# Performance work log

Measured on AMD Instinct MI355X. Metric: run time of the kernel, lower is better.

Reference implementation:

```python
import jax, jax.numpy as jnp
import numpy as np

PAD_IDX, SOS_IDX, EOS_IDX = 0, 1, 2
NEG = -10000.0
B, T, K = 512, 1024, 64


def setup_inputs() -> dict:
    key = jax.random.key(0)
    k1, k2 = jax.random.split(key)
    h = jax.random.normal(k1, (B, T, K), dtype=jnp.float32)
    trans = np.asarray(jax.random.normal(k2, (K, K), dtype=jnp.float32)).copy()
    # constraints applied in crf.__init__
    trans[SOS_IDX, :] = NEG
    trans[:, EOS_IDX] = NEG
    trans[:, PAD_IDX] = NEG
    trans[PAD_IDX, :] = NEG
    trans[PAD_IDX, EOS_IDX] = 0.0
    trans[PAD_IDX, PAD_IDX] = 0.0
    # gold tag sequences: y0[:,0]=SOS, real tags in [3,K), PAD after length
    rng = np.random.default_rng(0)
    lengths = rng.integers(T // 2, T + 1, size=B)
    y = rng.integers(3, K, size=(B, T + 1))
    y[:, 0] = SOS_IDX
    pos = np.arange(1, T + 1)[None, :]
    y[:, 1:] = np.where(pos <= lengths[:, None], y[:, 1:], PAD_IDX)
    return {"h": h, "trans": jnp.asarray(trans), "y0": jnp.asarray(y, dtype=jnp.int64)}


def reference(h, trans, y0):
    mask = (y0[:, 1:] > PAD_IDX).astype(h.dtype)  # [B,T]
    hm = h * mask[:, :, None]                      # rnn.forward masks emissions

    # ---- forward algorithm: log partition Z ----
    init = jnp.full((B, K), NEG, hm.dtype).at[:, SOS_IDX].set(0.0)

    def step(score, xs):
        h_t, m_t = xs  # [B,K], [B]
        # score_t[b, next, prev] = score[b, prev] + h_t[b, next] + trans[next, prev]
        s = jax.nn.logsumexp(score[:, None, :] + h_t[:, :, None] + trans[None], axis=2)
        m = m_t[:, None]
        return s * m + score * (1.0 - m), None

    score, _ = jax.lax.scan(step, init, (hm.transpose(1, 0, 2), mask.T))
    Z = jax.nn.logsumexp(score + trans[EOS_IDX], axis=1)  # [B]

    # ---- gold path score ----
    emit = jnp.take_along_axis(hm, y0[:, 1:, None], axis=2)[..., 0]  # [B,T]
    tr = trans[y0[:, 1:], y0[:, :-1]]                                 # [B,T]
    gold = jnp.sum((emit + tr) * mask, axis=1)
    last_idx = mask.sum(1).astype(jnp.int32)[:, None]                 # length L -> y0[:, L]
    last_tag = jnp.take_along_axis(y0, last_idx.astype(y0.dtype), axis=1)[:, 0]
    gold = gold + trans[EOS_IDX, last_tag]

    return jnp.mean(Z - gold)
```

## Files before the change

### kernel.cpp

```cpp
#include <hip/hip_runtime.h>


#define PAD_IDX 0
#define SOS_IDX 1
#define EOS_IDX 2
constexpr int B = 512, T = 1024, K = 64;
constexpr int REFL = 3;

__device__ __forceinline__ int yval(const int* __restrict__ y, int i, int sh) {
  return y[i << sh];
}

__global__ __launch_bounds__(256) void gold_len_kernel(
    const float* __restrict__ h, const float* __restrict__ trans,
    const int* __restrict__ y0, double* __restrict__ goldOut,
    int* __restrict__ lenOut)
{
  const int b = blockIdx.x, tid = threadIdx.x;
  const float* hb = h + (size_t)b * T * K;
  const int sh = (y0[1] == 0) ? 1 : 0;
  const int* yb = y0 + (((size_t)b * (T + 1)) << sh);

  double acc = 0.0;
  int maxpos = 0;
  for (int t = tid; t < T; t += 256) {
    int ycur = yval(yb, t + 1, sh);
    if (ycur > PAD_IDX) {
      int yprev = yval(yb, t, sh);
      acc += (double)(hb[(size_t)t * K + ycur] + trans[ycur * K + yprev]);
      maxpos = t + 1;
    }
  }
  #pragma unroll
  for (int off = 32; off > 0; off >>= 1) {
    acc += __shfl_down(acc, off, 64);
    maxpos = max(maxpos, __shfl_down(maxpos, off, 64));
  }
  __shared__ double sacc[4];
  __shared__ int smax[4];
  if ((tid & 63) == 0) { sacc[tid >> 6] = acc; smax[tid >> 6] = maxpos; }
  __syncthreads();
  if (tid == 0) {
    double a = (sacc[0] + sacc[1]) + (sacc[2] + sacc[3]);
    int len = max(max(smax[0], smax[1]), max(smax[2], smax[3]));
    int last = yval(yb, len, sh);
    a += (double)trans[EOS_IDX * K + last];
    goldOut[b] = a;
    lenOut[b] = len;
  }
}

__global__ __launch_bounds__(64) void fwd_kernel(
    const float* __restrict__ h, const float* __restrict__ trans,
    const int* __restrict__ lenIn, double* __restrict__ ZdOut)
{
  __shared__ alignas(16) float u_lds[K];
  const int b = blockIdx.x;
  const int k = threadIdx.x;
  const float* hb = h + (size_t)b * T * K;
  const int len = lenIn[b];

  float Er[K];
  #pragma unroll
  for (int j = 0; j < K; ++j) Er[j] = __expf(trans[k * K + j]);

  float u = (k == SOS_IDX) ? 1.0f : 0.0f;
  double O = 0.0;

  auto STEP = [&](float ehv, bool RN) {
    u_lds[k] = u;
    const float4* u4 = reinterpret_cast<const float4*>(u_lds);
    float a[8] = {0, 0, 0, 0, 0, 0, 0, 0};
    #pragma unroll
    for (int c = 0; c < 16; ++c) {
      float4 uu = u4[c];
      a[(4 * c + 0) & 7] = fmaf(Er[4 * c + 0], uu.x, a[(4 * c + 0) & 7]);
      a[(4 * c + 1) & 7] = fmaf(Er[4 * c + 1], uu.y, a[(4 * c + 1) & 7]);
      a[(4 * c + 2) & 7] = fmaf(Er[4 * c + 2], uu.z, a[(4 * c + 2) & 7]);
      a[(4 * c + 3) & 7] = fmaf(Er[4 * c + 3], uu.w, a[(4 * c + 3) & 7]);
    }
    float v = ((a[0] + a[4]) + (a[1] + a[5])) + ((a[2] + a[6]) + (a[3] + a[7]));
    if (RN) {
      float vr = __uint_as_float(__builtin_amdgcn_readlane(__float_as_uint(v), REFL));
      float rc = __builtin_amdgcn_rcpf(vr);
      O -= (double)__logf(rc);
      u = v * rc * ehv;
    } else {
      u = v * ehv;
    }
  };

  const int lm1 = len - 1;
  auto hload = [&](int t) { return hb[(size_t)min(t, lm1) * K + k]; };

  float p0 = hload(0), p1 = hload(1), p2 = hload(2), p3 = hload(3);
  int t = 0;
  for (; t + 4 <= len; t += 4) {
    float n0 = hload(t + 4), n1 = hload(t + 5), n2 = hload(t + 6), n3 = hload(t + 7);
    float e0 = __expf(p0), e1 = __expf(p1), e2 = __expf(p2), e3 = __expf(p3);
    STEP(e0, false); STEP(e1, true); STEP(e2, false); STEP(e3, true);
    p0 = n0; p1 = n1; p2 = n2; p3 = n3;
  }
  for (; t < len; ++t) STEP(__expf(hb[(size_t)t * K + k]), true);

  float w = u * __expf(trans[EOS_IDX * K + k]);
  #pragma unroll
  for (int off = 32; off > 0; off >>= 1) w += __shfl_xor(w, off, 64);
  if (k == 0) ZdOut[b] = O + (double)__logf(w);
}

__global__ __launch_bounds__(512) void reduce_kernel(
    const double* __restrict__ Zd, const double* __restrict__ goldIn,
    float* __restrict__ out)
{
  __shared__ double sdata[8];
  const int tid = threadIdx.x;
  double v = Zd[tid] - goldIn[tid];
  #pragma unroll
  for (int off = 32; off > 0; off >>= 1) v += __shfl_down(v, off, 64);
  if ((tid & 63) == 0) sdata[tid >> 6] = v;
  __syncthreads();
  if (tid == 0) {
    double s = 0.0;
    #pragma unroll
    for (int i = 0; i < 8; ++i) s += sdata[i];
    out[0] = (float)(s / (double)B);
  }
}

extern "C" void kernel_launch(void* const* d_in, const int* in_sizes, int n_in,
                              void* d_out, int out_size, void* d_ws, size_t ws_size,
                              hipStream_t stream) {
  const float* h = (const float*)d_in[0];
  const float* trans = (const float*)d_in[1];
  const int* y0 = (const int*)d_in[2];

  double* Zd = (double*)d_ws;
  double* gold = Zd + B;
  int* len = (int*)(gold + B);

  gold_len_kernel<<<B, 256, 0, stream>>>(h, trans, y0, gold, len);
  fwd_kernel<<<B, 64, 0, stream>>>(h, trans, len, Zd);
  reduce_kernel<<<1, 512, 0, stream>>>(Zd, gold, (float*)d_out);
}
```

Before: 447.0 us.

## Interleave two batch recurrences per wavefront with packed FMA and per-step renormalisation

The forward kernel now gives each 64-lane block two sequences and interleaves their recurrences so the two independent dependency chains hide each other's LDS and FMA latency. It uses packed v2f FMAs and renormalises on every step, guarding against a zero reference value. The gold kernel is widened to 1024 threads so each thread handles one timestep. The cost is half as many blocks and a serial tail for the longer of the two sequences.

```diff
diff --git a/kernel.cpp b/kernel.cpp
--- a/kernel.cpp
+++ b/kernel.cpp
@@ -7,11 +7,13 @@
 constexpr int B = 512, T = 1024, K = 64;
 constexpr int REFL = 3;
 
+typedef float v2f __attribute__((ext_vector_type(2)));
+
 __device__ __forceinline__ int yval(const int* __restrict__ y, int i, int sh) {
   return y[i << sh];
 }
 
-__global__ __launch_bounds__(256) void gold_len_kernel(
+__global__ __launch_bounds__(1024) void gold_len_kernel(
     const float* __restrict__ h, const float* __restrict__ trans,
     const int* __restrict__ y0, double* __restrict__ goldOut,
     int* __restrict__ lenOut)
@@ -21,92 +23,163 @@
   const int sh = (y0[1] == 0) ? 1 : 0;
   const int* yb = y0 + (((size_t)b * (T + 1)) << sh);
 
+  int ycur = yval(yb, tid + 1, sh);
   double acc = 0.0;
-  int maxpos = 0;
-  for (int t = tid; t < T; t += 256) {
-    int ycur = yval(yb, t + 1, sh);
-    if (ycur > PAD_IDX) {
-      int yprev = yval(yb, t, sh);
-      acc += (double)(hb[(size_t)t * K + ycur] + trans[ycur * K + yprev]);
-      maxpos = t + 1;
-    }
+  int mpos = 0;
+  if (ycur > PAD_IDX) {
+    int yprev = yval(yb, tid, sh);
+    acc = (double)(hb[(size_t)tid * K + ycur] + trans[ycur * K + yprev]);
+    mpos = tid + 1;
   }
   #pragma unroll
   for (int off = 32; off > 0; off >>= 1) {
     acc += __shfl_down(acc, off, 64);
-    maxpos = max(maxpos, __shfl_down(maxpos, off, 64));
-  }
-  __shared__ double sacc[4];
-  __shared__ int smax[4];
-  if ((tid & 63) == 0) { sacc[tid >> 6] = acc; smax[tid >> 6] = maxpos; }
+    mpos = max(mpos, __shfl_down(mpos, off, 64));
+  }
+  __shared__ double sa[16];
+  __shared__ int sm[16];
+  if ((tid & 63) == 0) { sa[tid >> 6] = acc; sm[tid >> 6] = mpos; }
   __syncthreads();
-  if (tid == 0) {
-    double a = (sacc[0] + sacc[1]) + (sacc[2] + sacc[3]);
-    int len = max(max(smax[0], smax[1]), max(smax[2], smax[3]));
-    int last = yval(yb, len, sh);
-    a += (double)trans[EOS_IDX * K + last];
-    goldOut[b] = a;
-    lenOut[b] = len;
-  }
-}
-
-__global__ __launch_bounds__(64) void fwd_kernel(
+  if (tid < 64) {
+    double a = (tid < 16) ? sa[tid] : 0.0;
+    int mp = (tid < 16) ? sm[tid] : 0;
+    #pragma unroll
+    for (int off = 8; off > 0; off >>= 1) {
+      a += __shfl_down(a, off, 64);
+      mp = max(mp, __shfl_down(mp, off, 64));
+    }
+    if (tid == 0) {
+      int last = yval(yb, mp, sh);
+      goldOut[b] = a + (double)trans[EOS_IDX * K + last];
+      lenOut[b] = mp;
+    }
+  }
+}
+
+__global__ __launch_bounds__(64) void fwd2_kernel(
     const float* __restrict__ h, const float* __restrict__ trans,
     const int* __restrict__ lenIn, double* __restrict__ ZdOut)
 {
-  __shared__ alignas(16) float u_lds[K];
-  const int b = blockIdx.x;
+  __shared__ alignas(16) float lds0[K];
+  __shared__ alignas(16) float lds1[K];
   const int k = threadIdx.x;
-  const float* hb = h + (size_t)b * T * K;
-  const int len = lenIn[b];
-
-  float Er[K];
+  const int b0 = 2 * blockIdx.x, b1 = b0 + 1;
+  const float* hb0 = h + (size_t)b0 * T * K;
+  const float* hb1 = h + (size_t)b1 * T * K;
+  const int len0 = lenIn[b0], len1 = lenIn[b1];
+
+  v2f E2[32];
   #pragma unroll
-  for (int j = 0; j < K; ++j) Er[j] = __expf(trans[k * K + j]);
-
-  float u = (k == SOS_IDX) ? 1.0f : 0.0f;
-  double O = 0.0;
-
-  auto STEP = [&](float ehv, bool RN) {
-    u_lds[k] = u;
-    const float4* u4 = reinterpret_cast<const float4*>(u_lds);
-    float a[8] = {0, 0, 0, 0, 0, 0, 0, 0};
+  for (int j = 0; j < 32; ++j) {
+    E2[j].x = __expf(trans[k * K + 2 * j]);
+    E2[j].y = __expf(trans[k * K + 2 * j + 1]);
+  }
+  const float eEOS = __expf(trans[EOS_IDX * K + k]);
+
+  float w0 = (k == SOS_IDX) ? 1.0f : 0.0f, w1 = w0;
+  double O0 = 0.0, O1 = 0.0;
+
+  auto RC = [&](float w) {
+    float wr = __uint_as_float(__builtin_amdgcn_readlane(__float_as_uint(w), REFL));
+    return wr > 0.0f ? __builtin_amdgcn_rcpf(wr) : 1.0f;
+  };
+
+  auto STEP2 = [&](float f0, float f1) {
+    lds0[k] = w0;
+    lds1[k] = w1;
+    float rc0 = RC(w0), rc1 = RC(w1);
+    float m0 = f0 * rc0, m1 = f1 * rc1;
+    O0 -= (double)__logf(rc0);
+    O1 -= (double)__logf(rc1);
+    const float4* u0 = reinterpret_cast<const float4*>(lds0);
+    const float4* u1 = reinterpret_cast<const float4*>(lds1);
+    v2f p0 = {0,0}, p1 = {0,0}, p2 = {0,0}, p3 = {0,0};
+    v2f q0 = {0,0}, q1 = {0,0}, q2 = {0,0}, q3 = {0,0};
     #pragma unroll
     for (int c = 0; c < 16; ++c) {
-      float4 uu = u4[c];
-      a[(4 * c + 0) & 7] = fmaf(Er[4 * c + 0], uu.x, a[(4 * c + 0) & 7]);
-      a[(4 * c + 1) & 7] = fmaf(Er[4 * c + 1], uu.y, a[(4 * c + 1) & 7]);
-      a[(4 * c + 2) & 7] = fmaf(Er[4 * c + 2], uu.z, a[(4 * c + 2) & 7]);
-      a[(4 * c + 3) & 7] = fmaf(Er[4 * c + 3], uu.w, a[(4 * c + 3) & 7]);
-    }
-    float v = ((a[0] + a[4]) + (a[1] + a[5])) + ((a[2] + a[6]) + (a[3] + a[7]));
-    if (RN) {
-      float vr = __uint_as_float(__builtin_amdgcn_readlane(__float_as_uint(v), REFL));
-      float rc = __builtin_amdgcn_rcpf(vr);
-      O -= (double)__logf(rc);
-      u = v * rc * ehv;
-    } else {
-      u = v * ehv;
-    }
-  };
-
-  const int lm1 = len - 1;
-  auto hload = [&](int t) { return hb[(size_t)min(t, lm1) * K + k]; };
-
-  float p0 = hload(0), p1 = hload(1), p2 = hload(2), p3 = hload(3);
+      float4 x0 = u0[c];
+      float4 x1 = u1[c];
+      v2f xa0 = {x0.x, x0.y}, xb0 = {x0.z, x0.w};
+      v2f xa1 = {x1.x, x1.y}, xb1 = {x1.z, x1.w};
+      if (c & 1) {
+        p2 = E2[2*c] * xa0 + p2;  p3 = E2[2*c+1] * xb0 + p3;
+        q2 = E2[2*c] * xa1 + q2;  q3 = E2[2*c+1] * xb1 + q3;
+      } else {
+        p0 = E2[2*c] * xa0 + p0;  p1 = E2[2*c+1] * xb0 + p1;
+        q0 = E2[2*c] * xa1 + q0;  q1 = E2[2*c+1] * xb1 + q1;
+      }
+    }
+    v2f sp = (p0 + p2) + (p1 + p3);
+    v2f sq = (q0 + q2) + (q1 + q3);
+    w0 = (sp.x + sp.y) * m0;
+    w1 = (sq.x + sq.y) * m1;
+  };
+
+  auto STEP1 = [&](float f, float& w, double& O) {
+    lds0[k] = w;
+    float rc = RC(w);
+    float m = f * rc;
+    O -= (double)__logf(rc);
+    const float4* u0 = reinterpret_cast<const float4*>(lds0);
+    v2f p0 = {0,0}, p1 = {0,0}, p2 = {0,0}, p3 = {0,0};
+    #pragma unroll
+    for (int c = 0; c < 16; ++c) {
+      float4 x0 = u0[c];
+      v2f xa0 = {x0.x, x0.y}, xb0 = {x0.z, x0.w};
+      if (c & 1) { p2 = E2[2*c] * xa0 + p2;  p3 = E2[2*c+1] * xb0 + p3; }
+      else       { p0 = E2[2*c] * xa0 + p0;  p1 = E2[2*c+1] * xb0 + p1; }
+    }
+    v2f sp = (p0 + p2) + (p1 + p3);
+    w = (sp.x + sp.y) * m;
+  };
+
+  auto EPI = [&](float w, double O, int b) {
+    float s = w * eEOS;
+    #pragma unroll
+    for (int off = 32; off > 0; off >>= 1) s += __shfl_xor(s, off, 64);
+    if (k == 0) ZdOut[b] = O + (double)__logf(s);
+  };
+
+  const int lmin = min(len0, len1), lmax = max(len0, len1);
+  const int lm1_0 = len0 - 1, lm1_1 = len1 - 1;
+  auto hl0 = [&](int t) { return hb0[(size_t)min(t, lm1_0) * K + k]; };
+  auto hl1 = [&](int t) { return hb1[(size_t)min(t, lm1_1) * K + k]; };
+
+  float p00 = hl0(0), p01 = hl0(1), p02 = hl0(2), p03 = hl0(3);
+  float p10 = hl1(0), p11 = hl1(1), p12 = hl1(2), p13 = hl1(3);
   int t = 0;
-  for (; t + 4 <= len; t += 4) {
-    float n0 = hload(t + 4), n1 = hload(t + 5), n2 = hload(t + 6), n3 = hload(t + 7);
-    float e0 = __expf(p0), e1 = __expf(p1), e2 = __expf(p2), e3 = __expf(p3);
-    STEP(e0, false); STEP(e1, true); STEP(e2, false); STEP(e3, true);
-    p0 = n0; p1 = n1; p2 = n2; p3 = n3;
-  }
-  for (; t < len; ++t) STEP(__expf(hb[(size_t)t * K + k]), true);
-
-  float w = u * __expf(trans[EOS_IDX * K + k]);
-  #pragma unroll
-  for (int off = 32; off > 0; off >>= 1) w += __shfl_xor(w, off, 64);
-  if (k == 0) ZdOut[b] = O + (double)__logf(w);
+  for (; t + 4 <= lmin; t += 4) {
+    float n00 = hl0(t+4), n01 = hl0(t+5), n02 = hl0(t+6), n03 = hl0(t+7);
+    float n10 = hl1(t+4), n11 = hl1(t+5), n12 = hl1(t+6), n13 = hl1(t+7);
+    STEP2(__expf(p00), __expf(p10));
+    STEP2(__expf(p01), __expf(p11));
+    STEP2(__expf(p02), __expf(p12));
+    STEP2(__expf(p03), __expf(p13));
+    p00 = n00; p01 = n01; p02 = n02; p03 = n03;
+    p10 = n10; p11 = n11; p12 = n12; p13 = n13;
+  }
+  for (; t < lmin; ++t) STEP2(__expf(hl0(t)), __expf(hl1(t)));
+
+  const bool sel0long = (len0 >= len1);
+  if (sel0long) EPI(w1, O1, b1); else EPI(w0, O0, b0);
+
+  const float* hbL = sel0long ? hb0 : hb1;
+  const int lenL = lmax, lm1L = lenL - 1;
+  float wL = sel0long ? w0 : w1;
+  double OL = sel0long ? O0 : O1;
+  auto hlL = [&](int tt) { return hbL[(size_t)min(tt, lm1L) * K + k]; };
+
+  float q0 = hlL(t), q1 = hlL(t + 1), q2 = hlL(t + 2), q3 = hlL(t + 3);
+  for (; t + 4 <= lenL; t += 4) {
+    float n0 = hlL(t+4), n1 = hlL(t+5), n2 = hlL(t+6), n3 = hlL(t+7);
+    STEP1(__expf(q0), wL, OL);
+    STEP1(__expf(q1), wL, OL);
+    STEP1(__expf(q2), wL, OL);
+    STEP1(__expf(q3), wL, OL);
+    q0 = n0; q1 = n1; q2 = n2; q3 = n3;
+  }
+  for (; t < lenL; ++t) STEP1(__expf(hlL(t)), wL, OL);
+  EPI(wL, OL, sel0long ? b0 : b1);
 }
 
 __global__ __launch_bounds__(512) void reduce_kernel(
@@ -139,7 +212,7 @@
   double* gold = Zd + B;
   int* len = (int*)(gold + B);
 
-  gold_len_kernel<<<B, 256, 0, stream>>>(h, trans, y0, gold, len);
-  fwd_kernel<<<B, 64, 0, stream>>>(h, trans, len, Zd);
+  gold_len_kernel<<<B, 1024, 0, stream>>>(h, trans, y0, gold, len);
+  fwd2_kernel<<<B / 2, 64, 0, stream>>>(h, trans, len, Zd);
   reduce_kernel<<<1, 512, 0, stream>>>(Zd, gold, (float*)d_out);
 }
```

After: 555.6 us. 24.3% more time.

## Broadcast forward state via readlane and packed FMA instead of LDS

Applied to the files above, without the earlier changes.

The forward recursion no longer round-trips the per-tag state through shared memory. Each step broadcasts all 64 lanes' values with readlane and accumulates with packed two-wide FMAs, and it normalizes every step using a lane that is read anyway. The gold/length kernel now uses 1024 threads, so each thread handles one timestep, and it reduces in two levels. The aim is to cut LDS write/read latency on the serial critical path. The cost is 64 scalar readlanes per step and a normalization on every step.

```diff
diff --git a/kernel.cpp b/kernel.cpp
--- a/kernel.cpp
+++ b/kernel.cpp
@@ -5,13 +5,18 @@
 #define SOS_IDX 1
 #define EOS_IDX 2
 constexpr int B = 512, T = 1024, K = 64;
-constexpr int REFL = 3;
+
+typedef float v2f __attribute__((ext_vector_type(2)));
+
+__device__ __forceinline__ float RL(float v, int lane) {
+  return __uint_as_float(__builtin_amdgcn_readlane(__float_as_uint(v), lane));
+}
 
 __device__ __forceinline__ int yval(const int* __restrict__ y, int i, int sh) {
   return y[i << sh];
 }
 
-__global__ __launch_bounds__(256) void gold_len_kernel(
+__global__ __launch_bounds__(1024) void gold_len_kernel(
     const float* __restrict__ h, const float* __restrict__ trans,
     const int* __restrict__ y0, double* __restrict__ goldOut,
     int* __restrict__ lenOut)
@@ -21,73 +26,78 @@
   const int sh = (y0[1] == 0) ? 1 : 0;
   const int* yb = y0 + (((size_t)b * (T + 1)) << sh);
 
+  int ycur = yval(yb, tid + 1, sh);
   double acc = 0.0;
-  int maxpos = 0;
-  for (int t = tid; t < T; t += 256) {
-    int ycur = yval(yb, t + 1, sh);
-    if (ycur > PAD_IDX) {
-      int yprev = yval(yb, t, sh);
-      acc += (double)(hb[(size_t)t * K + ycur] + trans[ycur * K + yprev]);
-      maxpos = t + 1;
-    }
+  int mpos = 0;
+  if (ycur > PAD_IDX) {
+    int yprev = yval(yb, tid, sh);
+    acc = (double)(hb[(size_t)tid * K + ycur] + trans[ycur * K + yprev]);
+    mpos = tid + 1;
   }
   #pragma unroll
   for (int off = 32; off > 0; off >>= 1) {
     acc += __shfl_down(acc, off, 64);
-    maxpos = max(maxpos, __shfl_down(maxpos, off, 64));
+    mpos = max(mpos, __shfl_down(mpos, off, 64));
   }
-  __shared__ double sacc[4];
-  __shared__ int smax[4];
-  if ((tid & 63) == 0) { sacc[tid >> 6] = acc; smax[tid >> 6] = maxpos; }
+  __shared__ double sa[16];
+  __shared__ int sm[16];
+  if ((tid & 63) == 0) { sa[tid >> 6] = acc; sm[tid >> 6] = mpos; }
   __syncthreads();
-  if (tid == 0) {
-    double a = (sacc[0] + sacc[1]) + (sacc[2] + sacc[3]);
-    int len = max(max(smax[0], smax[1]), max(smax[2], smax[3]));
-    int last = yval(yb, len, sh);
-    a += (double)trans[EOS_IDX * K + last];
-    goldOut[b] = a;
-    lenOut[b] = len;
+  if (tid < 64) {
+    double a = (tid < 16) ? sa[tid] : 0.0;
+    int mp = (tid < 16) ? sm[tid] : 0;
+    #pragma unroll
+    for (int off = 8; off > 0; off >>= 1) {
+      a += __shfl_down(a, off, 64);
+      mp = max(mp, __shfl_down(mp, off, 64));
+    }
+    if (tid == 0) {
+      int last = yval(yb, mp, sh);
+      goldOut[b] = a + (double)trans[EOS_IDX * K + last];
+      lenOut[b] = mp;
+    }
   }
 }
 
-__global__ __launch_bounds__(64) void fwd_kernel(
+__global__ __launch_bounds__(64) void fwd_rl_kernel(
     const float* __restrict__ h, const float* __restrict__ trans,
     const int* __restrict__ lenIn, double* __restrict__ ZdOut)
 {
-  __shared__ alignas(16) float u_lds[K];
+  const int k = threadIdx.x;
   const int b = blockIdx.x;
-  const int k = threadIdx.x;
   const float* hb = h + (size_t)b * T * K;
   const int len = lenIn[b];
 
-  float Er[K];
+  v2f E2[32];
   #pragma unroll
-  for (int j = 0; j < K; ++j) Er[j] = __expf(trans[k * K + j]);
+  for (int j = 0; j < 32; ++j) {
+    E2[j].x = __expf(trans[k * K + 2 * j]);
+    E2[j].y = __expf(trans[k * K + 2 * j + 1]);
+  }
+  const float eEOS = __expf(trans[EOS_IDX * K + k]);
 
-  float u = (k == SOS_IDX) ? 1.0f : 0.0f;
+  float w = (k == SOS_IDX) ? 1.0f : 0.0f;
   double O = 0.0;
 
-  auto STEP = [&](float ehv, bool RN) {
-    u_lds[k] = u;
-    const float4* u4 = reinterpret_cast<const float4*>(u_lds);
-    float a[8] = {0, 0, 0, 0, 0, 0, 0, 0};
+  auto STEP = [&](float f) {
+    v2f a0 = {0, 0}, a1 = {0, 0}, a2 = {0, 0}, a3 = {0, 0};
+    float s3 = 0.0f;
     #pragma unroll
-    for (int c = 0; c < 16; ++c) {
-      float4 uu = u4[c];
-      a[(4 * c + 0) & 7] = fmaf(Er[4 * c + 0], uu.x, a[(4 * c + 0) & 7]);
-      a[(4 * c + 1) & 7] = fmaf(Er[4 * c + 1], uu.y, a[(4 * c + 1) & 7]);
-      a[(4 * c + 2) & 7] = fmaf(Er[4 * c + 2], uu.z, a[(4 * c + 2) & 7]);
-      a[(4 * c + 3) & 7] = fmaf(Er[4 * c + 3], uu.w, a[(4 * c + 3) & 7]);
+    for (int j = 0; j < 32; ++j) {
+      v2f s;
+      s.x = RL(w, 2 * j);
+      s.y = RL(w, 2 * j + 1);
+      if (j == 1) s3 = s.y;
+      if ((j & 3) == 0)      a0 = E2[j] * s + a0;
+      else if ((j & 3) == 1) a1 = E2[j] * s + a1;
+      else if ((j & 3) == 2) a2 = E2[j] * s + a2;
+      else                   a3 = E2[j] * s + a3;
     }
-    float v = ((a[0] + a[4]) + (a[1] + a[5])) + ((a[2] + a[6]) + (a[3] + a[7]));
-    if (RN) {
-      float vr = __uint_as_float(__builtin_amdgcn_readlane(__float_as_uint(v), REFL));
-      float rc = __builtin_amdgcn_rcpf(vr);
-      O -= (double)__logf(rc);
-      u = v * rc * ehv;
-    } else {
-      u = v * ehv;
-    }
+    v2f sv = (a0 + a1) + (a2 + a3);
+    float v = sv.x + sv.y;
+    float rc = (s3 > 0.0f) ? __builtin_amdgcn_rcpf(s3) : 1.0f;
+    O -= (double)__logf(rc);
+    w = v * (f * rc);
   };
 
   const int lm1 = len - 1;
@@ -97,16 +107,15 @@
   int t = 0;
   for (; t + 4 <= len; t += 4) {
     float n0 = hload(t + 4), n1 = hload(t + 5), n2 = hload(t + 6), n3 = hload(t + 7);
-    float e0 = __expf(p0), e1 = __expf(p1), e2 = __expf(p2), e3 = __expf(p3);
-    STEP(e0, false); STEP(e1, true); STEP(e2, false); STEP(e3, true);
+    STEP(__expf(p0)); STEP(__expf(p1)); STEP(__expf(p2)); STEP(__expf(p3));
     p0 = n0; p1 = n1; p2 = n2; p3 = n3;
   }
-  for (; t < len; ++t) STEP(__expf(hb[(size_t)t * K + k]), true);
+  for (; t < len; ++t) STEP(__expf(hb[(size_t)t * K + k]));
 
-  float w = u * __expf(trans[EOS_IDX * K + k]);
+  float s = w * eEOS;
   #pragma unroll
-  for (int off = 32; off > 0; off >>= 1) w += __shfl_xor(w, off, 64);
-  if (k == 0) ZdOut[b] = O + (double)__logf(w);
+  for (int off = 32; off > 0; off >>= 1) s += __shfl_xor(s, off, 64);
+  if (k == 0) ZdOut[b] = O + (double)__logf(s);
 }
 
 __global__ __launch_bounds__(512) void reduce_kernel(
@@ -139,7 +148,7 @@
   double* gold = Zd + B;
   int* len = (int*)(gold + B);
 
-  gold_len_kernel<<<B, 256, 0, stream>>>(h, trans, y0, gold, len);
-  fwd_kernel<<<B, 64, 0, stream>>>(h, trans, len, Zd);
+  gold_len_kernel<<<B, 1024, 0, stream>>>(h, trans, y0, gold, len);
+  fwd_rl_kernel<<<B, 64, 0, stream>>>(h, trans, len, Zd);
   reduce_kernel<<<1, 512, 0, stream>>>(Zd, gold, (float*)d_out);
 }
```

Result: slower. 558.8 us (+25.0%).
